# Performance work log

Hardware: AMD Instinct MI355X
Metric: run time of the kernel (lower is better)

## Reference

```python
import jax, jax.numpy as jnp
import numpy as np

U, I, D = 100000, 100000, 64
B, T = 16384, 1_638_400
R = 5  # rating levels 1..5


def setup_inputs() -> dict:
    key = jax.random.key(0)
    ks = jax.random.split(key, 8)
    return {
        "user_idx": jax.random.randint(ks[0], (B,), 0, U, dtype=jnp.int32),
        "item_idx": jax.random.randint(ks[1], (B,), 0, I, dtype=jnp.int32),
        "flat_items": jax.random.randint(ks[2], (T,), 0, I, dtype=jnp.int32),
        "seg_ids": jnp.sort(jax.random.randint(ks[3], (T,), 0, B * R, dtype=jnp.int32)),
        "user_emb": (jax.random.uniform(ks[4], (U, D), dtype=jnp.float32) - 0.5) * 0.01,
        "item_emb": (jax.random.uniform(ks[5], (I, D), dtype=jnp.float32) - 0.5) * 0.01,
        "Mr": (jax.random.uniform(ks[6], (I, D), dtype=jnp.float32) - 0.5) * 0.01,
        "user_bias": jnp.zeros((U,), dtype=jnp.float32),
        "item_bias": jnp.zeros((I,), dtype=jnp.float32),
        "global_avg": jnp.float32(3.5),
    }


def reference(user_idx, item_idx, flat_items, seg_ids, user_emb, item_emb, Mr, user_bias, item_bias, global_avg):
    num_seg = B * R  # segment = sample_i * 5 + (rating - 1)
    # Original torch code does Mr_ik(rate_dict).sum() -> scalar over ALL dims,
    # then broadcasts that scalar onto the latent_dim vector UuMpc[i].
    row_sum = Mr[flat_items].sum(axis=-1)  # [T] per-item full-row sum
    # Emulate `rate_dict.remove(item_idx[i])`: mask out the target item of this sample.
    match = flat_items == item_idx[seg_ids // R]  # [T]
    contrib = jnp.where(match, 0.0, row_sum)
    seg_sum = jax.ops.segment_sum(contrib, seg_ids, num_segments=num_seg)  # [B*5]
    cnt = jax.ops.segment_sum(jnp.where(match, 0.0, 1.0), seg_ids, num_segments=num_seg)
    per_seg = jnp.where(cnt > 0, seg_sum / jnp.sqrt(jnp.maximum(cnt, 1.0)), 0.0)
    uu_mpc = per_seg.reshape(B, R).sum(axis=-1)  # [B] scalar per sample
    user_vec = user_emb[user_idx] + uu_mpc[:, None]  # broadcast scalar over latent dim
    item_vec = item_emb[item_idx]
    rui = (user_vec * item_vec).sum(axis=-1) + user_bias[user_idx] + item_bias[item_idx] + global_avg
    return jnp.clip(rui, 1.0, 5.0)
```

## Files before the change

### kernel.cpp

```cpp
#include <hip/hip_runtime.h>

#define U_N 100000
#define I_N 100000
#define D_N 64
#define B_N 16384
#define T_N 1638400
#define R_N 5

__global__ void rowsum_kernel(const float* __restrict__ Mr, float* __restrict__ rowsum) {
    int tid = blockIdx.x * blockDim.x + threadIdx.x;
    int row = tid >> 4;
    int sub = tid & 15;
    if (row >= I_N) return;
    const float4* p = (const float4*)(Mr + (long)row * D_N);
    float4 v4 = p[sub];
    float v = v4.x + v4.y + v4.z + v4.w;
    v += __shfl_xor(v, 1);
    v += __shfl_xor(v, 2);
    v += __shfl_xor(v, 4);
    v += __shfl_xor(v, 8);
    if (sub == 0) rowsum[row] = v;
}

__device__ __forceinline__ int lower_bound_i(const int* __restrict__ a, int n, int val) {
    int lo = 0, hi = n;
    while (lo < hi) {
        int mid = (lo + hi) >> 1;
        if (a[mid] < val) lo = mid + 1; else hi = mid;
    }
    return lo;
}

__global__ void sample_kernel(const int* __restrict__ user_idx,
                              const int* __restrict__ item_idx,
                              const int* __restrict__ flat_items,
                              const int* __restrict__ seg_ids,
                              const float* __restrict__ user_emb,
                              const float* __restrict__ item_emb,
                              const float* __restrict__ user_bias,
                              const float* __restrict__ item_bias,
                              const float* __restrict__ global_avg,
                              const float* __restrict__ rowsum,
                              float* __restrict__ out) {
    __shared__ float s_sum[4][5];
    __shared__ int   s_cnt[4][5];

    int w    = threadIdx.x >> 6;
    int lane = threadIdx.x & 63;
    int b    = blockIdx.x * 4 + w;
    if (b >= B_N) return;

    if (lane < R_N) { s_sum[w][lane] = 0.f; s_cnt[w][lane] = 0; }
    __syncthreads();

    int lo = lower_bound_i(seg_ids, T_N, b * R_N);
    int hi = lower_bound_i(seg_ids, T_N, b * R_N + R_N);
    int target = item_idx[b];

    for (int t = lo + lane; t < hi; t += 64) {
        int sg = seg_ids[t];
        int it = flat_items[t];
        if (it != target) {
            int r = sg - b * R_N;
            atomicAdd(&s_sum[w][r], rowsum[it]);
            atomicAdd(&s_cnt[w][r], 1);
        }
    }
    __syncthreads();

    float uu = 0.f;
    if (lane == 0) {
        #pragma unroll
        for (int r = 0; r < R_N; ++r) {
            int c = s_cnt[w][r];
            if (c > 0) uu += s_sum[w][r] / sqrtf((float)c);
        }
    }

    int u = user_idx[b];
    float ue = user_emb[(long)u * D_N + lane];
    float ie = item_emb[(long)target * D_N + lane];
    float dot = ue * ie;
    float isum = ie;
    #pragma unroll
    for (int off = 32; off >= 1; off >>= 1) {
        dot  += __shfl_xor(dot, off);
        isum += __shfl_xor(isum, off);
    }
    if (lane == 0) {
        float rui = dot + uu * isum + user_bias[u] + item_bias[target] + global_avg[0];
        rui = fminf(fmaxf(rui, 1.0f), 5.0f);
        out[b] = rui;
    }
}

extern "C" void kernel_launch(void* const* d_in, const int* in_sizes, int n_in,
                              void* d_out, int out_size, void* d_ws, size_t ws_size,
                              hipStream_t stream) {
    const int*   user_idx   = (const int*)d_in[0];
    const int*   item_idx   = (const int*)d_in[1];
    const int*   flat_items = (const int*)d_in[2];
    const int*   seg_ids    = (const int*)d_in[3];
    const float* user_emb   = (const float*)d_in[4];
    const float* item_emb   = (const float*)d_in[5];
    const float* Mr         = (const float*)d_in[6];
    const float* user_bias  = (const float*)d_in[7];
    const float* item_bias  = (const float*)d_in[8];
    const float* global_avg = (const float*)d_in[9];
    float* out = (float*)d_out;

    float* rowsum = (float*)d_ws;

    rowsum_kernel<<<(I_N * 16 + 255) / 256, 256, 0, stream>>>(Mr, rowsum);
    sample_kernel<<<B_N / 4, 256, 0, stream>>>(
        user_idx, item_idx, flat_items, seg_ids, user_emb, item_emb,
        user_bias, item_bias, global_avg, rowsum, out);
}
```

Before: 166.5 us.

## Replace per-sample binary searches with precomputed sample start offsets

Adds a boundary-detection pass, fused into the rowsum kernel, that scans the sorted seg_ids and writes a start offset for every sample into workspace. The sample kernel then reads lo/hi directly instead of running two ~21-step binary searches over the 1.6M-element seg_ids array in every wavefront. This trades the dependent search loads for one extra streaming read of seg_ids and a scattered write of the offset array.

```diff
diff --git a/kernel.cpp b/kernel.cpp
--- a/kernel.cpp
+++ b/kernel.cpp
@@ -7,28 +7,47 @@
 #define T_N 1638400
 #define R_N 5
 
-__global__ void rowsum_kernel(const float* __restrict__ Mr, float* __restrict__ rowsum) {
-    int tid = blockIdx.x * blockDim.x + threadIdx.x;
-    int row = tid >> 4;
-    int sub = tid & 15;
-    if (row >= I_N) return;
-    const float4* p = (const float4*)(Mr + (long)row * D_N);
-    float4 v4 = p[sub];
-    float v = v4.x + v4.y + v4.z + v4.w;
-    v += __shfl_xor(v, 1);
-    v += __shfl_xor(v, 2);
-    v += __shfl_xor(v, 4);
-    v += __shfl_xor(v, 8);
-    if (sub == 0) rowsum[row] = v;
-}
+#define RS_THREADS (I_N * 16)
+#define BD_THREADS (T_N / 4)
+#define K1_THREADS (RS_THREADS + BD_THREADS)
 
-__device__ __forceinline__ int lower_bound_i(const int* __restrict__ a, int n, int val) {
-    int lo = 0, hi = n;
-    while (lo < hi) {
-        int mid = (lo + hi) >> 1;
-        if (a[mid] < val) lo = mid + 1; else hi = mid;
+__global__ void prep_kernel(const float* __restrict__ Mr,
+                            const int* __restrict__ seg_ids,
+                            float* __restrict__ rowsum,
+                            int* __restrict__ sample_start) {
+    int gtid = blockIdx.x * blockDim.x + threadIdx.x;
+    if (gtid < RS_THREADS) {
+        int row = gtid >> 4;
+        int sub = gtid & 15;
+        const float4* p = (const float4*)(Mr + (long)row * D_N);
+        float4 v4 = p[sub];
+        float v = v4.x + v4.y + v4.z + v4.w;
+        v += __shfl_xor(v, 1);
+        v += __shfl_xor(v, 2);
+        v += __shfl_xor(v, 4);
+        v += __shfl_xor(v, 8);
+        if (sub == 0) rowsum[row] = v;
+    } else {
+        int t4 = gtid - RS_THREADS;
+        if (t4 >= BD_THREADS) return;
+        int base = t4 * 4;
+        int4 s4 = ((const int4*)seg_ids)[t4];
+        int sv[5];
+        sv[0] = (base == 0) ? -1 : seg_ids[base - 1];
+        sv[1] = s4.x; sv[2] = s4.y; sv[3] = s4.z; sv[4] = s4.w;
+        #pragma unroll
+        for (int j = 0; j < 4; ++j) {
+            int sp = sv[j], sc = sv[j + 1];
+            if (sc > sp) {
+                int b_lo = (sp + 5) / 5;
+                int b_hi = sc / 5;
+                for (int b = b_lo; b <= b_hi; ++b) sample_start[b] = base + j;
+            }
+        }
+        if (base + 4 == T_N) {
+            for (int b = sv[4] / 5 + 1; b <= B_N; ++b) sample_start[b] = T_N;
+        }
     }
-    return lo;
 }
 
 __global__ void sample_kernel(const int* __restrict__ user_idx,
@@ -41,6 +60,7 @@
                               const float* __restrict__ item_bias,
                               const float* __restrict__ global_avg,
                               const float* __restrict__ rowsum,
+                              const int* __restrict__ sample_start,
                               float* __restrict__ out) {
     __shared__ float s_sum[4][5];
     __shared__ int   s_cnt[4][5];
@@ -53,8 +73,8 @@
     if (lane < R_N) { s_sum[w][lane] = 0.f; s_cnt[w][lane] = 0; }
     __syncthreads();
 
-    int lo = lower_bound_i(seg_ids, T_N, b * R_N);
-    int hi = lower_bound_i(seg_ids, T_N, b * R_N + R_N);
+    int lo = sample_start[b];
+    int hi = sample_start[b + 1];
     int target = item_idx[b];
 
     for (int t = lo + lane; t < hi; t += 64) {
@@ -109,10 +129,12 @@
     const float* global_avg = (const float*)d_in[9];
     float* out = (float*)d_out;
 
-    float* rowsum = (float*)d_ws;
+    float* rowsum       = (float*)d_ws;
+    int*   sample_start = (int*)(rowsum + I_N);
 
-    rowsum_kernel<<<(I_N * 16 + 255) / 256, 256, 0, stream>>>(Mr, rowsum);
+    prep_kernel<<<(K1_THREADS + 255) / 256, 256, 0, stream>>>(
+        Mr, seg_ids, rowsum, sample_start);
     sample_kernel<<<B_N / 4, 256, 0, stream>>>(
         user_idx, item_idx, flat_items, seg_ids, user_emb, item_emb,
-        user_bias, item_bias, global_avg, rowsum, out);
+        user_bias, item_bias, global_avg, rowsum, sample_start, out);
 }
```

New measurement: 147.3 us. 11.5% less time.
